# Kernel tuning notes

Hardware: AMD Instinct MI355X
Metric: run time of the kernel (lower is better)

Reference implementation:

```python
import jax, jax.numpy as jnp
import numpy as np

# Static discretization grid (torch version computes this on host from data;
# with inputs in [0,1) the clamps min(..,-2)-0.1 / max(..,2)+0.1 make it constant).
PPU = 128          # points_per_unit
MULT = 16          # 2 ** rho.num_halving_layers
XMIN, XMAX = -2.1, 2.1
NUM_GRID = int(np.ceil(PPU * (XMAX - XMIN) / MULT) * MULT)  # 544
SIGMA_CH = 1024
RHO_C = 8          # rho in/out channels


def setup_inputs() -> dict:
    key = jax.random.key(0)
    ks = jax.random.split(key, 8)
    B, N, M = 8, 2048, 2048
    log_ls = float(np.log(2.0 / PPU))  # init_length_scale = 2 / points_per_unit
    return {
        "x": jax.random.uniform(ks[0], (B, N, 1), dtype=jnp.float32),
        "y": jax.random.normal(ks[1], (B, N, 1), dtype=jnp.float32),
        "x_out": jax.random.uniform(ks[2], (B, M, 1), dtype=jnp.float32),
        # encoder ConvDeepSet (in_channels = 2: density + y)
        "enc_sigma": jnp.full((2,), log_ls, dtype=jnp.float32),
        "enc_W": jax.random.normal(ks[3], (2, RHO_C), dtype=jnp.float32) * 0.5,
        "enc_b": jnp.zeros((RHO_C,), dtype=jnp.float32),
        # rho stand-in: point-wise linear 8 -> 8
        "rho_W": jax.random.normal(ks[4], (RHO_C, RHO_C), dtype=jnp.float32) * 0.35,
        "rho_b": jnp.zeros((RHO_C,), dtype=jnp.float32),
        # mean FinalLayer (in_channels = rho.out_channels = 8, out_channels = 1)
        "mean_sigma": jnp.full((RHO_C,), log_ls, dtype=jnp.float32),
        "mean_W": jax.random.normal(ks[5], (RHO_C, 1), dtype=jnp.float32) * 0.35,
        "mean_b": jnp.zeros((1,), dtype=jnp.float32),
        # sigma FinalLayer (out_channels = sigma_channels = 1024)
        "sig_sigma": jnp.full((RHO_C,), log_ls, dtype=jnp.float32),
        "sig_W": jax.random.normal(ks[6], (RHO_C, SIGMA_CH), dtype=jnp.float32) * 0.35,
        "sig_b": jnp.zeros((SIGMA_CH,), dtype=jnp.float32),
        "noise_scale": jnp.zeros((1,), dtype=jnp.float32),
    }


def _rbf_weights(a, t, log_sigma):
    # a: (B, n, 1), t: (B, m, 1) -> (B, n, m, C) per-channel RBF weights
    d = (a - jnp.swapaxes(t, 1, 2)) ** 2            # (B, n, m) squared dists
    scales = jnp.exp(log_sigma)                      # (C,)
    return jnp.exp(-0.5 * d[..., None] / scales ** 2)


def reference(x, y, x_out, enc_sigma, enc_W, enc_b, rho_W, rho_b,
              mean_sigma, mean_W, mean_b, sig_sigma, sig_W, sig_b, noise_scale):
    B = x.shape[0]
    grid = jnp.broadcast_to(
        jnp.linspace(XMIN, XMAX, NUM_GRID, dtype=x.dtype)[None, :, None],
        (B, NUM_GRID, 1))

    # --- encoder ConvDeepSet: density channel + value channel, RBF smoothing onto grid
    wt = _rbf_weights(x, grid, enc_sigma)            # (B, N, G, 2)
    y_aug = jnp.concatenate([jnp.ones_like(x), y], axis=-1)  # (B, N, 2)
    F = jnp.einsum('bnc,bngc->bgc', y_aug, wt)       # (B, G, 2)
    den, conv = F[..., :1], F[..., 1:]
    F = jnp.concatenate([den, conv / (den + 1e-8)], axis=-1)
    h = jax.nn.sigmoid(F @ enc_W + enc_b)            # (B, G, 8)

    # --- rho (stand-in point-wise linear CNN)
    h = h @ rho_W + rho_b                            # (B, G, 8)

    # --- mean FinalLayer: RBF set-conv from grid to x_out, then linear
    wt_m = _rbf_weights(grid, x_out, mean_sigma)     # (B, G, M, 8)
    mean = jnp.einsum('bgc,bgmc->bmc', h, wt_m) @ mean_W + mean_b  # (B, M, 1)

    # --- sigma FinalLayer -> basis embedding, inner-product covariance
    wt_s = _rbf_weights(grid, x_out, sig_sigma)      # (B, G, M, 8)
    basis = jnp.einsum('bgc,bgmc->bmc', h, wt_s) @ sig_W + sig_b   # (B, M, 1024)
    cov = jnp.einsum('bmc,bnc->bmn', basis, basis)   # (B, M, M)
    cov = cov + jnp.exp(noise_scale[0]) * jnp.eye(cov.shape[-1], dtype=cov.dtype)
    return mean, cov
```

## Files before the change

kernel.cpp:

```cpp
#include <hip/hip_runtime.h>
#include <math.h>

#define GRID_N 544
#define BATCH  8
#define NPTS   2048
#define MPTS   2048
#define XMIN_F (-2.1f)
#define STEP_F (4.2f / 543.0f)

typedef float v4f __attribute__((ext_vector_type(4)));

#define PRM_OFF 0
#define H_OFF   128
#define FST_OFF (H_OFF + BATCH*GRID_N*8)
#define P_OFF   (FST_OFF + BATCH*8*MPTS)
#define CM_OFF  (P_OFF + BATCH*MPTS*8)

__global__ __launch_bounds__(256) void k_encode(
    const float* __restrict__ x, const float* __restrict__ y,
    const float* __restrict__ enc_sigma,
    const float* __restrict__ enc_W, const float* __restrict__ enc_b,
    const float* __restrict__ rho_W, const float* __restrict__ rho_b,
    const float* __restrict__ mean_sigma, const float* __restrict__ sig_sigma,
    const float* __restrict__ sig_W, const float* __restrict__ sig_b,
    float* __restrict__ prm, float* __restrict__ h_out) {
  int b = blockIdx.y, g = blockIdx.x, t = threadIdx.x;

  if (g == GRID_N) {
    if (b != 0) return;
    __shared__ float part[256];
    {
      int pair = t >> 2, q = t & 3;
      int i = pair >> 3, j = pair & 7;
      float s = 0.f;
      int k0 = q * 256;
      for (int k = k0; k < k0 + 256; ++k) s += sig_W[i*1024+k] * sig_W[j*1024+k];
      part[t] = s;
      __syncthreads();
      if (q == 0) prm[16 + pair] = part[t] + part[t+1] + part[t+2] + part[t+3];
      __syncthreads();
    }
    {
      int ch = t >> 5, lane = t & 31;
      float s = 0.f;
      for (int k = lane; k < 1024; k += 32) s += sig_W[ch*1024+k] * sig_b[k];
      part[t] = s;
      __syncthreads();
      if (lane == 0) {
        float acc = 0.f;
        for (int k = 0; k < 32; ++k) acc += part[(ch<<5)+k];
        prm[80 + ch] = acc;
      }
      __syncthreads();
    }
    if (t < 32) {
      float v = 0.f;
      for (int k = t; k < 1024; k += 32) v += sig_b[k] * sig_b[k];
      part[t] = v;
    }
    __syncthreads();
    if (t == 0) {
      float v = 0.f;
      for (int k = 0; k < 32; ++k) v += part[k];
      prm[88] = v;
    } else if (t == 1) {
      bool f = true;
      for (int c = 0; c < 8; ++c) {
        prm[c]     = 0.5f * __expf(-2.f * mean_sigma[c]);
        prm[8 + c] = 0.5f * __expf(-2.f * sig_sigma[c]);
        if (mean_sigma[c] != mean_sigma[0] || sig_sigma[c] != sig_sigma[0]) f = false;
      }
      if (mean_sigma[0] != sig_sigma[0]) f = false;
      prm[89] = f ? 1.f : 0.f;
    }
    return;
  }

  float gv = XMIN_F + (float)g * STEP_F;
  float es0 = enc_sigma[0], es1 = enc_sigma[1];
  float a0 = 0.5f * __expf(-2.f * es0);
  float a1 = 0.5f * __expf(-2.f * es1);
  bool uni = (es0 == es1);
  const float4* x4 = (const float4*)(x + (size_t)b * NPTS);
  const float4* y4 = (const float4*)(y + (size_t)b * NPTS);
  float s0 = 0.f, s1 = 0.f;
  #pragma unroll
  for (int i = 0; i < 2; ++i) {
    int n = i * 256 + t;
    float4 xv = x4[n], yv = y4[n];
    float dx, d, w;
    dx = xv.x - gv; d = dx*dx; w = __expf(-d*a0); s0 += w;
    s1 += yv.x * (uni ? w : __expf(-d*a1));
    dx = xv.y - gv; d = dx*dx; w = __expf(-d*a0); s0 += w;
    s1 += yv.y * (uni ? w : __expf(-d*a1));
    dx = xv.z - gv; d = dx*dx; w = __expf(-d*a0); s0 += w;
    s1 += yv.z * (uni ? w : __expf(-d*a1));
    dx = xv.w - gv; d = dx*dx; w = __expf(-d*a0); s0 += w;
    s1 += yv.w * (uni ? w : __expf(-d*a1));
  }
  #pragma unroll
  for (int off = 32; off > 0; off >>= 1) {
    s0 += __shfl_down(s0, off);
    s1 += __shfl_down(s1, off);
  }
  __shared__ float w0s[4], w1s[4];
  int wid = t >> 6;
  if ((t & 63) == 0) { w0s[wid] = s0; w1s[wid] = s1; }
  __syncthreads();
  if (t == 0) {
    float den = w0s[0] + w0s[1] + w0s[2] + w0s[3];
    float conv = w1s[0] + w1s[1] + w1s[2] + w1s[3];
    float F0 = den, F1 = conv / (den + 1e-8f);
    float hh[8];
    #pragma unroll
    for (int jj = 0; jj < 8; ++jj) {
      float z = F0 * enc_W[jj] + F1 * enc_W[8 + jj] + enc_b[jj];
      hh[jj] = 1.f / (1.f + __expf(-z));
    }
    #pragma unroll
    for (int jj = 0; jj < 8; ++jj) {
      float v = rho_b[jj];
      #pragma unroll
      for (int ii = 0; ii < 8; ++ii) v += hh[ii] * rho_W[ii*8 + jj];
      h_out[((size_t)b * GRID_N + g) * 8 + jj] = v;
    }
  }
}

__global__ __launch_bounds__(256) void k_feat(
    const float* __restrict__ x_out, const float* __restrict__ mean_W,
    const float* __restrict__ mean_b, const float* __restrict__ prm,
    const float* __restrict__ h, float* __restrict__ mean_out,
    float* __restrict__ fSt, float* __restrict__ Pv, float* __restrict__ cm) {
  int b = blockIdx.y, t = threadIdx.x;
  int ml = t & 63, slice = t >> 6;
  int m = blockIdx.x * 64 + ml;
  float xo = x_out[(size_t)b * MPTS + m];
  bool fused = prm[89] != 0.f;
  float accm[8] = {0,0,0,0,0,0,0,0};
  float accs[8] = {0,0,0,0,0,0,0,0};
  const float* hb = h + (size_t)b * GRID_N * 8;
  const float4* h4 = (const float4*)hb;
  int gbase = slice * 136;
  if (fused) {
    float a = prm[0];
    for (int gg = 0; gg < 136; ++gg) {
      int g = gbase + gg;
      float gv = XMIN_F + (float)g * STEP_F;
      float dx = gv - xo;
      float w = __expf(-(dx*dx) * a);
      float4 h0 = h4[g*2], h1 = h4[g*2+1];
      accm[0] += h0.x * w; accm[1] += h0.y * w;
      accm[2] += h0.z * w; accm[3] += h0.w * w;
      accm[4] += h1.x * w; accm[5] += h1.y * w;
      accm[6] += h1.z * w; accm[7] += h1.w * w;
    }
  } else {
    float am[8], asg[8];
    #pragma unroll
    for (int c = 0; c < 8; ++c) { am[c] = prm[c]; asg[c] = prm[8 + c]; }
    for (int gg = 0; gg < 136; ++gg) {
      int g = gbase + gg;
      float gv = XMIN_F + (float)g * STEP_F;
      float dx = gv - xo;
      float d = dx * dx;
      #pragma unroll
      for (int c = 0; c < 8; ++c) {
        float hv = hb[g*8 + c];
        accm[c] += hv * __expf(-d * am[c]);
        accs[c] += hv * __expf(-d * asg[c]);
      }
    }
  }
  __shared__ float red[256 * 17];
  #pragma unroll
  for (int c = 0; c < 8; ++c) {
    red[t*17 + c] = accm[c];
    if (!fused) red[t*17 + 8 + c] = accs[c];
  }
  __syncthreads();
  if (t < 64) {
    int mm = blockIdx.x * 64 + t;
    float fm[8], fs[8];
    #pragma unroll
    for (int c = 0; c < 8; ++c) {
      fm[c] = red[t*17+c] + red[(t+64)*17+c] + red[(t+128)*17+c] + red[(t+192)*17+c];
    }
    if (fused) {
      #pragma unroll
      for (int c = 0; c < 8; ++c) fs[c] = fm[c];
    } else {
      #pragma unroll
      for (int c = 0; c < 8; ++c) {
        fs[c] = red[t*17+8+c] + red[(t+64)*17+8+c] + red[(t+128)*17+8+c] + red[(t+192)*17+8+c];
      }
    }
    float mv = mean_b[0];
    #pragma unroll
    for (int c = 0; c < 8; ++c) mv += fm[c] * mean_W[c];
    mean_out[(size_t)b * MPTS + mm] = mv;
    float cmv = prm[88];
    #pragma unroll
    for (int c = 0; c < 8; ++c) cmv += fs[c] * prm[80 + c];
    cm[(size_t)b * MPTS + mm] = cmv;
    size_t base = ((size_t)b * MPTS + mm) * 8;
    #pragma unroll
    for (int c2 = 0; c2 < 8; ++c2) {
      float p = prm[80 + c2];
      #pragma unroll
      for (int c = 0; c < 8; ++c) p += fs[c] * prm[16 + c*8 + c2];
      Pv[base + c2] = p;
    }
    float* fp = fSt + (size_t)b * 8 * MPTS + mm;
    #pragma unroll
    for (int c = 0; c < 8; ++c) fp[c * MPTS] = fs[c];
  }
}

__global__ __launch_bounds__(256) void k_cov(
    const float* __restrict__ fSt, const float* __restrict__ Pv,
    const float* __restrict__ cm, const float* __restrict__ noise_scale,
    float* __restrict__ cov) {
  int b = blockIdx.y, t = threadIdx.x;
  int half = blockIdx.x & 1, rt = blockIdx.x >> 1;
  int col = half * 1024 + 4 * t;
  int row0 = rt * 8;
  float noise = __expf(noise_scale[0]);
  v4f fn[8];
  const float* fb = fSt + (size_t)b * 8 * MPTS;
  #pragma unroll
  for (int c = 0; c < 8; ++c)
    fn[c] = *(const v4f*)(fb + c * MPTS + col);
  const float* Pr = Pv + ((size_t)b * MPTS + row0) * 8;
  const float* Cr = cm + (size_t)b * MPTS + row0;
  v4f o[8];
  #pragma unroll
  for (int i = 0; i < 8; ++i) {
    float cc = Cr[i];
    float a0 = cc, a1 = cc, a2 = cc, a3 = cc;
    #pragma unroll
    for (int c = 0; c < 8; ++c) {
      float p = Pr[i * 8 + c];
      a0 += p * fn[c].x; a1 += p * fn[c].y;
      a2 += p * fn[c].z; a3 += p * fn[c].w;
    }
    int mg = row0 + i;
    if (mg == col)     a0 += noise;
    if (mg == col + 1) a1 += noise;
    if (mg == col + 2) a2 += noise;
    if (mg == col + 3) a3 += noise;
    o[i].x = a0; o[i].y = a1; o[i].z = a2; o[i].w = a3;
  }
  #pragma unroll
  for (int i = 0; i < 8; ++i) {
    v4f* dst = (v4f*)(cov + ((size_t)b * MPTS + row0 + i) * MPTS + col);
    __builtin_nontemporal_store(o[i], dst);
  }
}

extern "C" void kernel_launch(void* const* d_in, const int* in_sizes, int n_in,
                              void* d_out, int out_size, void* d_ws, size_t ws_size,
                              hipStream_t stream) {
  const float* x          = (const float*)d_in[0];
  const float* y          = (const float*)d_in[1];
  const float* x_out      = (const float*)d_in[2];
  const float* enc_sigma  = (const float*)d_in[3];
  const float* enc_W      = (const float*)d_in[4];
  const float* enc_b      = (const float*)d_in[5];
  const float* rho_W      = (const float*)d_in[6];
  const float* rho_b      = (const float*)d_in[7];
  const float* mean_sigma = (const float*)d_in[8];
  const float* mean_W     = (const float*)d_in[9];
  const float* mean_b     = (const float*)d_in[10];
  const float* sig_sigma  = (const float*)d_in[11];
  const float* sig_W      = (const float*)d_in[12];
  const float* sig_b      = (const float*)d_in[13];
  const float* noise_sc   = (const float*)d_in[14];

  float* wsf = (float*)d_ws;
  float* prm  = wsf + PRM_OFF;
  float* hbuf = wsf + H_OFF;
  float* fStb = wsf + FST_OFF;
  float* Pb   = wsf + P_OFF;
  float* cmb  = wsf + CM_OFF;

  float* mean_out = (float*)d_out;
  float* cov_out  = mean_out + (size_t)BATCH * MPTS;

  k_encode<<<dim3(GRID_N + 1, BATCH), 256, 0, stream>>>(
      x, y, enc_sigma, enc_W, enc_b, rho_W, rho_b,
      mean_sigma, sig_sigma, sig_W, sig_b, prm, hbuf);
  k_feat<<<dim3(MPTS/64, BATCH), 256, 0, stream>>>(x_out, mean_W, mean_b, prm,
                                                   hbuf, mean_out, fStb, Pb, cmb);
  k_cov<<<dim3(2 * (MPTS/8), BATCH), 256, 0, stream>>>(fStb, Pb, cmb, noise_sc,
                                                       cov_out);
}
```

Measured before the change: 211.1 us.

## Stage x/y in LDS and compute 8 grid points per encode block

The encode kernel now launches 68 compute blocks per batch instead of 544. Each block loads the batch's x and y into shared memory once, and each wave computes two grid points with a single wave-level reduction. This replaces redundant global loads of x/y per grid point and the cross-wave shared reduction. The cost is fewer blocks (68×8) and a serial loop of two grid points per wave, which may lower parallelism on a large GPU.

Result: no change. 211.8 us (+0.3%).

```diff
diff --git a/kernel.cpp b/kernel.cpp
--- a/kernel.cpp
+++ b/kernel.cpp
@@ -15,6 +15,7 @@
 #define FST_OFF (H_OFF + BATCH*GRID_N*8)
 #define P_OFF   (FST_OFF + BATCH*8*MPTS)
 #define CM_OFF  (P_OFF + BATCH*MPTS*8)
+
 
 __global__ __launch_bounds__(256) void k_encode(
     const float* __restrict__ x, const float* __restrict__ y,
@@ -24,9 +25,9 @@
     const float* __restrict__ mean_sigma, const float* __restrict__ sig_sigma,
     const float* __restrict__ sig_W, const float* __restrict__ sig_b,
     float* __restrict__ prm, float* __restrict__ h_out) {
-  int b = blockIdx.y, g = blockIdx.x, t = threadIdx.x;
-
-  if (g == GRID_N) {
+  int b = blockIdx.y, gt = blockIdx.x, t = threadIdx.x;
+
+  if (gt == 68) {
     if (b != 0) return;
     __shared__ float part[256];
     {
@@ -76,53 +77,63 @@
     return;
   }
 
-  float gv = XMIN_F + (float)g * STEP_F;
+  __shared__ float xs[NPTS], ys[NPTS];
+  {
+    const float4* x4 = (const float4*)(x + (size_t)b * NPTS);
+    const float4* y4 = (const float4*)(y + (size_t)b * NPTS);
+    float4* xs4 = (float4*)xs;
+    float4* ys4 = (float4*)ys;
+    #pragma unroll
+    for (int i = 0; i < 2; ++i) {
+      int n = i * 256 + t;
+      xs4[n] = x4[n];
+      ys4[n] = y4[n];
+    }
+  }
+  __syncthreads();
+
   float es0 = enc_sigma[0], es1 = enc_sigma[1];
   float a0 = 0.5f * __expf(-2.f * es0);
   float a1 = 0.5f * __expf(-2.f * es1);
   bool uni = (es0 == es1);
-  const float4* x4 = (const float4*)(x + (size_t)b * NPTS);
-  const float4* y4 = (const float4*)(y + (size_t)b * NPTS);
-  float s0 = 0.f, s1 = 0.f;
-  #pragma unroll
-  for (int i = 0; i < 2; ++i) {
-    int n = i * 256 + t;
-    float4 xv = x4[n], yv = y4[n];
-    float dx, d, w;
-    dx = xv.x - gv; d = dx*dx; w = __expf(-d*a0); s0 += w;
-    s1 += yv.x * (uni ? w : __expf(-d*a1));
-    dx = xv.y - gv; d = dx*dx; w = __expf(-d*a0); s0 += w;
-    s1 += yv.y * (uni ? w : __expf(-d*a1));
-    dx = xv.z - gv; d = dx*dx; w = __expf(-d*a0); s0 += w;
-    s1 += yv.z * (uni ? w : __expf(-d*a1));
-    dx = xv.w - gv; d = dx*dx; w = __expf(-d*a0); s0 += w;
-    s1 += yv.w * (uni ? w : __expf(-d*a1));
-  }
-  #pragma unroll
-  for (int off = 32; off > 0; off >>= 1) {
-    s0 += __shfl_down(s0, off);
-    s1 += __shfl_down(s1, off);
-  }
-  __shared__ float w0s[4], w1s[4];
-  int wid = t >> 6;
-  if ((t & 63) == 0) { w0s[wid] = s0; w1s[wid] = s1; }
-  __syncthreads();
-  if (t == 0) {
-    float den = w0s[0] + w0s[1] + w0s[2] + w0s[3];
-    float conv = w1s[0] + w1s[1] + w1s[2] + w1s[3];
-    float F0 = den, F1 = conv / (den + 1e-8f);
-    float hh[8];
-    #pragma unroll
-    for (int jj = 0; jj < 8; ++jj) {
-      float z = F0 * enc_W[jj] + F1 * enc_W[8 + jj] + enc_b[jj];
-      hh[jj] = 1.f / (1.f + __expf(-z));
-    }
-    #pragma unroll
-    for (int jj = 0; jj < 8; ++jj) {
-      float v = rho_b[jj];
-      #pragma unroll
-      for (int ii = 0; ii < 8; ++ii) v += hh[ii] * rho_W[ii*8 + jj];
-      h_out[((size_t)b * GRID_N + g) * 8 + jj] = v;
+  int wave = t >> 6, lane = t & 63;
+
+  #pragma unroll 1
+  for (int gi = 0; gi < 2; ++gi) {
+    int g = gt * 8 + wave * 2 + gi;
+    float gv = XMIN_F + (float)g * STEP_F;
+    float s0 = 0.f, s1 = 0.f;
+    #pragma unroll 4
+    for (int k = 0; k < 32; ++k) {
+      int n = lane + (k << 6);
+      float xv = xs[n], yv = ys[n];
+      float dx = xv - gv;
+      float d = dx * dx;
+      float w = __expf(-d * a0);
+      s0 += w;
+      s1 += yv * (uni ? w : __expf(-d * a1));
+    }
+    #pragma unroll
+    for (int off = 32; off > 0; off >>= 1) {
+      s0 += __shfl_down(s0, off);
+      s1 += __shfl_down(s1, off);
+    }
+    if (lane == 0) {
+      float den = s0;
+      float F0 = den, F1 = s1 / (den + 1e-8f);
+      float hh[8];
+      #pragma unroll
+      for (int jj = 0; jj < 8; ++jj) {
+        float z = F0 * enc_W[jj] + F1 * enc_W[8 + jj] + enc_b[jj];
+        hh[jj] = 1.f / (1.f + __expf(-z));
+      }
+      #pragma unroll
+      for (int jj = 0; jj < 8; ++jj) {
+        float v = rho_b[jj];
+        #pragma unroll
+        for (int ii = 0; ii < 8; ++ii) v += hh[ii] * rho_W[ii*8 + jj];
+        h_out[((size_t)b * GRID_N + g) * 8 + jj] = v;
+      }
     }
   }
 }
@@ -287,7 +298,7 @@
   float* mean_out = (float*)d_out;
   float* cov_out  = mean_out + (size_t)BATCH * MPTS;
 
-  k_encode<<<dim3(GRID_N + 1, BATCH), 256, 0, stream>>>(
+  k_encode<<<dim3(69, BATCH), 256, 0, stream>>>(
       x, y, enc_sigma, enc_W, enc_b, rho_W, rho_b,
       mean_sigma, sig_sigma, sig_W, sig_b, prm, hbuf);
   k_feat<<<dim3(MPTS/64, BATCH), 256, 0, stream>>>(x_out, mean_W, mean_b, prm,
```
